# Optimization experiments

Hardware: AMD Instinct MI355X
Metric: run time of the kernel (lower is better)

The kernel has to match this reference:

```python
import jax, jax.numpy as jnp
import numpy as np

B, S, D, H, HD = 2, 4096, 768, 12, 64
W = 256  # one-sided attention window (attention_window=512 // 2)
SCALE = 1.0 / np.sqrt(HD).astype(np.float32)
NEG = -1e9


def setup_inputs() -> dict:
    key = jax.random.key(0)
    ks = jax.random.split(key, 13)
    inp = {"hidden_states": jax.random.normal(ks[0], (B, S, D), dtype=jnp.float32)}
    names = ["Wq", "Wk", "Wv", "Wqg", "Wkg", "Wvg"]
    for i, n in enumerate(names):
        inp[n] = jax.random.normal(ks[1 + i], (D, D), dtype=jnp.float32) * 0.02
        inp["b" + n[1:]] = jax.random.normal(ks[7 + i], (D,), dtype=jnp.float32) * 0.02
    inp["num_global"] = 32
    return inp


def _heads(x):
    # [B,S,D] -> [B,H,S,HD]
    return x.reshape(B, S, H, HD).transpose(0, 2, 1, 3)


def longformer_attn(hidden_states, Wq, bq, Wk, bk, Wv, bv, Wqg, bqg, Wkg, bkg, Wvg, bvg, G):
    q = _heads(hidden_states @ Wq + bq) * SCALE
    k = _heads(hidden_states @ Wk + bk)
    v = _heads(hidden_states @ Wv + bv)

    nc = S // W  # number of query chunks
    # --- banded (sliding window) scores via overlapping key chunks of size 3W ---
    Qc = q.reshape(B, H, nc, W, HD)
    kpad = jnp.pad(k, ((0, 0), (0, 0), (W, W), (0, 0)))
    win_idx = jnp.arange(nc)[:, None] * W + jnp.arange(3 * W)[None, :]  # [nc, 3W]
    K3 = kpad[:, :, win_idx]  # [B,H,nc,3W,HD]
    band = jnp.einsum('bhcqd,bhckd->bhcqk', Qc, K3)  # [B,H,nc,W,3W]
    # mask: key abs position in range, and relative offset within [-W, W]
    c = jnp.arange(nc)[:, None, None]
    pq = jnp.arange(W)[None, :, None]
    e = jnp.arange(3 * W)[None, None, :]
    kabs = c * W + e - W
    valid = (kabs >= 0) & (kabs < S) & (e >= pq) & (e <= pq + 2 * W)
    band = jnp.where(valid[None, None], band, NEG).reshape(B, H, S, 3 * W)

    # --- all queries also attend to the G global keys (regular key proj) ---
    sg = jnp.einsum('bhsd,bhgd->bhsg', q, k[:, :, :G])  # [B,H,S,G]
    probs = jax.nn.softmax(jnp.concatenate([sg, band], axis=-1), axis=-1)
    pg, pb = probs[..., :G], probs[..., G:].reshape(B, H, nc, W, 3 * W)

    vpad = jnp.pad(v, ((0, 0), (0, 0), (W, W), (0, 0)))
    V3 = vpad[:, :, win_idx]  # [B,H,nc,3W,HD]
    out = jnp.einsum('bhcqk,bhckd->bhcqd', pb, V3).reshape(B, H, S, HD)
    out = out + jnp.einsum('bhsg,bhgd->bhsd', pg, v[:, :, :G])

    # --- global queries attend to ALL tokens with the *_global projections ---
    qg = _heads(hidden_states @ Wqg + bqg)[:, :, :G] * SCALE  # [B,H,G,HD]
    kgf = _heads(hidden_states @ Wkg + bkg)
    vgf = _heads(hidden_states @ Wvg + bvg)
    gp = jax.nn.softmax(jnp.einsum('bhgd,bhsd->bhgs', qg, kgf), axis=-1)
    gout = jnp.einsum('bhgs,bhsd->bhgd', gp, vgf)  # [B,H,G,HD]
    out = out.at[:, :, :G].set(gout)

    return out.transpose(0, 2, 1, 3).reshape(B, S, D)


def reference(hidden_states, Wq, bq, Wk, bk, Wv, bv, Wqg, bqg, Wkg, bkg, Wvg, bvg, num_global):
    return longformer_attn(hidden_states, Wq, bq, Wk, bk, Wv, bv, Wqg, bqg, Wkg, bkg, Wvg, bvg, int(num_global))
```

## Files before the change

### kernel.cpp

```cpp
#include <hip/hip_runtime.h>
#include <hip/hip_bf16.h>


#define DEVI __device__ __forceinline__
typedef _Float16 f16;
typedef _Float16 h4 __attribute__((ext_vector_type(4)));
typedef _Float16 f16x8 __attribute__((ext_vector_type(8)));
typedef __attribute__((ext_vector_type(4))) float float4v;

DEVI float4v mfma16(f16x8 a, f16x8 b, float4v c) {
    return __builtin_amdgcn_mfma_f32_16x16x32_f16(a, b, c, 0, 0, 0);
}

DEVI void gl_lds16(const f16* g, f16* l) {
    __builtin_amdgcn_global_load_lds(
        (const __attribute__((address_space(1))) unsigned int*)g,
        (__attribute__((address_space(3))) unsigned int*)l, 16, 0, 0);
}

__global__ __launch_bounds__(256) void xcast(const float* __restrict__ x,
                                             f16* __restrict__ xh) {
    int i = (blockIdx.x * 256 + threadIdx.x) * 4;
    float4 v = *(const float4*)&x[i];
    h4 o = {(f16)v.x, (f16)v.y, (f16)v.z, (f16)v.w};
    *(h4*)&xh[i] = o;
}

__global__ __launch_bounds__(256) void wprep(
    const float* __restrict__ w0, const float* __restrict__ w1,
    const float* __restrict__ w2, const float* __restrict__ w3,
    const float* __restrict__ w4, const float* __restrict__ w5,
    f16* __restrict__ wt) {
    __shared__ float tile[64][65];
    int i = blockIdx.z;
    const float* W = (i == 0) ? w0 : (i == 1) ? w1 : (i == 2) ? w2
                   : (i == 3) ? w3 : (i == 4) ? w4 : w5;
    int n0 = blockIdx.x * 64, k0 = blockIdx.y * 64;
    int tx = threadIdx.x & 63, ty = threadIdx.x >> 6;
#pragma unroll
    for (int yy = 0; yy < 64; yy += 4)
        tile[yy + ty][tx] = W[(size_t)(k0 + yy + ty) * 768 + n0 + tx];
    __syncthreads();
#pragma unroll
    for (int yy = 0; yy < 64; yy += 4)
        wt[(size_t)(i * 768 + n0 + yy + ty) * 768 + k0 + tx] = (f16)tile[tx][yy + ty];
}

__global__ __launch_bounds__(256) void qkv_mfma3(
    const f16* __restrict__ Xh, const f16* __restrict__ Wt,
    const float* __restrict__ b0, const float* __restrict__ b1,
    const float* __restrict__ b2, const float* __restrict__ b3,
    const float* __restrict__ b4, const float* __restrict__ b5,
    f16* __restrict__ q, f16* __restrict__ k, f16* __restrict__ vT,
    f16* __restrict__ qg, f16* __restrict__ kg, f16* __restrict__ vgT) {
    constexpr int CLD = 136;
    __shared__ __align__(16) f16 At[128 * 32];
    __shared__ __align__(16) f16 Bt[128 * 32];
    __shared__ __align__(16) f16 Cl[128 * CLD];
    int tid = threadIdx.x, lane = tid & 63, wid = tid >> 6;
    int quad = lane >> 4, l15 = lane & 15;
    int m0 = blockIdx.x * 128;
    int wm = (wid >> 1) * 64, wn = (wid & 1) * 64;
    const f16* arow0 = Xh + (size_t)m0 * 768;
    const f16* brow0 = Wt + (size_t)blockIdx.y * 128 * 768;

    float4v acc[4][4];
#pragma unroll
    for (int mt = 0; mt < 4; ++mt)
#pragma unroll
        for (int nt = 0; nt < 4; ++nt) acc[mt][nt] = (float4v){0.f, 0.f, 0.f, 0.f};

    int s0 = tid, s1 = tid + 256;
    int r0 = s0 >> 2, o0 = (s0 & 3) * 8;
    int r1 = s1 >> 2, o1 = (s1 & 3) * 8;
    f16* ldsA0 = &At[wid * 512];
    f16* ldsB0 = &Bt[wid * 512];
    f16* ldsA1 = &At[2048 + wid * 512];
    f16* ldsB1 = &Bt[2048 + wid * 512];
    for (int kt = 0; kt < 24; ++kt) {
        int k0 = kt * 32;
        __syncthreads();
        gl_lds16(&arow0[(size_t)r0 * 768 + k0 + o0], ldsA0);
        gl_lds16(&brow0[(size_t)r0 * 768 + k0 + o0], ldsB0);
        gl_lds16(&arow0[(size_t)r1 * 768 + k0 + o1], ldsA1);
        gl_lds16(&brow0[(size_t)r1 * 768 + k0 + o1], ldsB1);
        __syncthreads();
        f16x8 af[4], bf[4];
#pragma unroll
        for (int mt = 0; mt < 4; ++mt)
            af[mt] = *(const f16x8*)&At[(wm + mt * 16 + l15) * 32 + quad * 8];
#pragma unroll
        for (int nt = 0; nt < 4; ++nt)
            bf[nt] = *(const f16x8*)&Bt[(wn + nt * 16 + l15) * 32 + quad * 8];
#pragma unroll
        for (int mt = 0; mt < 4; ++mt)
#pragma unroll
            for (int nt = 0; nt < 4; ++nt) acc[mt][nt] = mfma16(af[mt], bf[nt], acc[mt][nt]);
    }

    int grp = blockIdx.y / 6;
    const float* Bsel = (grp == 0) ? b0 : (grp == 1) ? b1 : (grp == 2) ? b2
                      : (grp == 3) ? b3 : (grp == 4) ? b4 : b5;
    int nb = (blockIdx.y - grp * 6) * 128;
    int b = m0 >> 12;
    bool tr = (grp == 2 || grp == 5);

    if (tr) {
#pragma unroll
        for (int nt = 0; nt < 4; ++nt) {
            float bias = Bsel[nb + wn + nt * 16 + l15];
#pragma unroll
            for (int mt = 0; mt < 4; ++mt) {
                float4v a = acc[mt][nt];
                h4 pk = {(f16)(a[0] + bias), (f16)(a[1] + bias),
                         (f16)(a[2] + bias), (f16)(a[3] + bias)};
                *(h4*)&Cl[(wn + nt * 16 + l15) * CLD + wm + mt * 16 + quad * 4] = pk;
            }
        }
    } else {
        float scale = (grp == 0 || grp == 3) ? 0.125f : 1.0f;
#pragma unroll
        for (int nt = 0; nt < 4; ++nt) {
            float bias = Bsel[nb + wn + nt * 16 + l15];
#pragma unroll
            for (int mt = 0; mt < 4; ++mt) {
                float4v a = acc[mt][nt];
#pragma unroll
                for (int r = 0; r < 4; ++r)
                    Cl[(wm + mt * 16 + quad * 4 + r) * CLD + wn + nt * 16 + l15] =
                        (f16)((a[r] + bias) * scale);
            }
        }
    }
    __syncthreads();

    if (tr) {
        f16* base = (grp == 2) ? vT : vgT;
        int c = tid & 127, sh = (tid >> 7) * 64;
        int ncol = nb + c, h = ncol >> 6, hd = ncol & 63;
        f16* dst = &base[((size_t)((b * 12 + h) * 64 + hd)) * 4096 + (m0 & 4095) + sh];
        const f16* src = &Cl[c * CLD + sh];
#pragma unroll
        for (int i = 0; i < 8; ++i)
            *(f16x8*)&dst[i * 8] = *(const f16x8*)&src[i * 8];
    } else {
        int sl = tid & 127, hh = tid >> 7;
        int s = (m0 & 4095) + sl;
        int h = (nb + hh * 64) >> 6;
        const f16* src = &Cl[sl * CLD + hh * 64];
        f16* dst = nullptr;
        if (grp == 3) {
            if (s < 32) dst = &qg[((size_t)((b * 12 + h) * 32 + s)) * 64];
        } else {
            f16* baseb = (grp == 0) ? q : (grp == 1) ? k : kg;
            dst = &baseb[((size_t)((b * 12 + h) * 4096 + s)) * 64];
        }
        if (dst)
#pragma unroll
            for (int i = 0; i < 8; ++i)
                *(f16x8*)&dst[i * 8] = *(const f16x8*)&src[i * 8];
    }
}

__global__ __launch_bounds__(256, 3) void band_mfma5(
    const f16* __restrict__ q, const f16* __restrict__ k, const f16* __restrict__ vT,
    float* __restrict__ out) {
    constexpr int LDK = 72, LDV = 136, LDP = 40;
    __shared__ __align__(16) f16 Kt[128 * LDK];
    __shared__ __align__(16) f16 Vt[64 * LDV];
    __shared__ __align__(16) f16 Pt[4][32 * LDP];
    int tid = threadIdx.x, lane = tid & 63, wid = tid >> 6;
    int quad = lane >> 4, l15 = lane & 15;
    int c = blockIdx.x & 31, h = (blockIdx.x >> 5) % 12, b = blockIdx.x / 384;
    const f16* qsl = q + (size_t)(b * 12 + h) * 4096 * 64;
    const f16* ksl = k + (size_t)(b * 12 + h) * 4096 * 64;
    const f16* vsl = vT + (size_t)(b * 12 + h) * 64 * 4096;
    int q0 = c * 128;
    int pq0 = q0 + wid * 32;

    f16x8 qf[2][2];
#pragma unroll
    for (int qg = 0; qg < 2; ++qg)
#pragma unroll
        for (int ks = 0; ks < 2; ++ks)
            qf[qg][ks] = *(const f16x8*)&qsl[(size_t)(pq0 + qg * 16 + l15) * 64 +
                                             ks * 32 + quad * 8];

    float4v Ot[4][2];
#pragma unroll
    for (int dt = 0; dt < 4; ++dt)
#pragma unroll
        for (int qg = 0; qg < 2; ++qg) Ot[dt][qg] = (float4v){0.f, 0.f, 0.f, 0.f};
    float lacc[2] = {0.f, 0.f};
    f16* PW = &Pt[wid][0];

    {
#pragma unroll
        for (int jt = 0; jt < 2; ++jt) {
            f16x8 kf0 = *(const f16x8*)&ksl[(size_t)(jt * 16 + l15) * 64 + quad * 8];
            f16x8 kf1 = *(const f16x8*)&ksl[(size_t)(jt * 16 + l15) * 64 + 32 + quad * 8];
#pragma unroll
            for (int qg = 0; qg < 2; ++qg) {
                float4v sacc = (float4v){0.f, 0.f, 0.f, 0.f};
                sacc = mfma16(kf0, qf[qg][0], sacc);
                sacc = mfma16(kf1, qf[qg][1], sacc);
                float p0 = __expf(sacc[0]), p1 = __expf(sacc[1]);
                float p2 = __expf(sacc[2]), p3 = __expf(sacc[3]);
                lacc[qg] += (p0 + p1) + (p2 + p3);
                h4 pk = {(f16)p0, (f16)p1, (f16)p2, (f16)p3};
                *(h4*)&PW[(qg * 16 + l15) * LDP + jt * 16 + quad * 4] = pk;
            }
        }
        f16x8 pf0 = *(const f16x8*)&PW[l15 * LDP + quad * 8];
        f16x8 pf1 = *(const f16x8*)&PW[(16 + l15) * LDP + quad * 8];
#pragma unroll
        for (int dt = 0; dt < 4; ++dt) {
            f16x8 vf = *(const f16x8*)&vsl[(size_t)(dt * 16 + l15) * 4096 + quad * 8];
            Ot[dt][0] = mfma16(vf, pf0, Ot[dt][0]);
            Ot[dt][1] = mfma16(vf, pf1, Ot[dt][1]);
        }
    }

    for (int r = 0; r < 5; ++r) {
        int kb = q0 - 256 + r * 128;
        if (kb < 0 || kb >= 4096) continue;
        __syncthreads();
        {
            int kr = tid >> 1, ko = (tid & 1) * 32;
            const f16* ks2 = &ksl[(size_t)(kb + kr) * 64 + ko];
            f16* kd = &Kt[kr * LDK + ko];
#pragma unroll
            for (int i = 0; i < 4; ++i) *(f16x8*)&kd[i * 8] = *(const f16x8*)&ks2[i * 8];
            int vr = tid >> 2, vo = (tid & 3) * 32;
            const f16* vs2 = &vsl[(size_t)vr * 4096 + kb + vo];
            f16* vd = &Vt[vr * LDV + vo];
#pragma unroll
            for (int i = 0; i < 4; ++i) *(f16x8*)&vd[i * 8] = *(const f16x8*)&vs2[i * 8];
        }
        __syncthreads();

        if (kb + 127 < pq0 - 256 || kb > pq0 + 287) continue;

#pragma unroll
        for (int tt = 0; tt < 2; ++tt) {
            int tb = kb + tt * 64;
            if (tb + 63 < pq0 - 256 || tb > pq0 + 287) continue;
#pragma unroll
            for (int hf = 0; hf < 2; ++hf) {
#pragma unroll
                for (int jt = 0; jt < 2; ++jt) {
                    int jl = tt * 64 + hf * 32 + jt * 16;
                    f16x8 kf0 = *(const f16x8*)&Kt[(jl + l15) * LDK + quad * 8];
                    f16x8 kf1 = *(const f16x8*)&Kt[(jl + l15) * LDK + 32 + quad * 8];
                    int j0 = kb + jl;
#pragma unroll
                    for (int qg = 0; qg < 2; ++qg) {
                        int qlo = pq0 + qg * 16;
                        h4 pk = {(f16)0.f, (f16)0.f, (f16)0.f, (f16)0.f};
                        bool dead = (j0 < qlo - 271) || (j0 > qlo + 271);
                        if (!dead) {
                            float4v sacc = (float4v){0.f, 0.f, 0.f, 0.f};
                            sacc = mfma16(kf0, qf[qg][0], sacc);
                            sacc = mfma16(kf1, qf[qg][1], sacc);
                            float p[4];
                            bool full = (j0 >= qlo - 241) && (j0 <= qlo + 241);
                            if (full) {
#pragma unroll
                                for (int rr = 0; rr < 4; ++rr) p[rr] = __expf(sacc[rr]);
                            } else {
#pragma unroll
                                for (int rr = 0; rr < 4; ++rr) {
                                    int d = (j0 + quad * 4 + rr) - (qlo + l15);
                                    p[rr] = ((unsigned)(d + 256) <= 512u) ? __expf(sacc[rr]) : 0.f;
                                }
                            }
                            lacc[qg] += (p[0] + p[1]) + (p[2] + p[3]);
                            pk = (h4){(f16)p[0], (f16)p[1], (f16)p[2], (f16)p[3]};
                        }
                        *(h4*)&PW[(qg * 16 + l15) * LDP + jt * 16 + quad * 4] = pk;
                    }
                }
                f16x8 pf0 = *(const f16x8*)&PW[l15 * LDP + quad * 8];
                f16x8 pf1 = *(const f16x8*)&PW[(16 + l15) * LDP + quad * 8];
#pragma unroll
                for (int dt = 0; dt < 4; ++dt) {
                    f16x8 vf = *(const f16x8*)&Vt[(dt * 16 + l15) * LDV +
                                                  tt * 64 + hf * 32 + quad * 8];
                    Ot[dt][0] = mfma16(vf, pf0, Ot[dt][0]);
                    Ot[dt][1] = mfma16(vf, pf1, Ot[dt][1]);
                }
            }
        }
    }

#pragma unroll
    for (int qg = 0; qg < 2; ++qg) {
        float lsum = lacc[qg];
        lsum += __shfl_xor(lsum, 16);
        lsum += __shfl_xor(lsum, 32);
        float inv = 1.f / lsum;
        size_t orow = (size_t)(b * 4096 + pq0 + qg * 16 + l15) * 768 + h * 64;
#pragma unroll
        for (int dt = 0; dt < 4; ++dt) {
            float4 o4 = {Ot[dt][qg][0] * inv, Ot[dt][qg][1] * inv,
                         Ot[dt][qg][2] * inv, Ot[dt][qg][3] * inv};
            *(float4*)&out[orow + dt * 16 + quad * 4] = o4;
        }
    }
}

__global__ __launch_bounds__(256) void global_part(
    const f16* __restrict__ qg, const f16* __restrict__ kg, const f16* __restrict__ vgT,
    float* __restrict__ Opart, float* __restrict__ Lpart) {
    constexpr int LDP = 72;
    __shared__ __align__(16) f16 Pt[4][32 * LDP];
    __shared__ __align__(16) float Osh[4][64 * 32];
    __shared__ float Lsh[4][32];
    int tid = threadIdx.x, lane = tid & 63, wid = tid >> 6;
    int quad = lane >> 4, l15 = lane & 15;
    int sl = blockIdx.x & 7, bh = blockIdx.x >> 3;
    const f16* qsl = qg + (size_t)bh * 32 * 64;
    const f16* ksl = kg + (size_t)bh * 4096 * 64;
    const f16* vsl = vgT + (size_t)bh * 64 * 4096;
    int kbase = sl * 512 + wid * 128;

    f16x8 qf[2][2];
#pragma unroll
    for (int g = 0; g < 2; ++g)
#pragma unroll
        for (int ks = 0; ks < 2; ++ks)
            qf[g][ks] = *(const f16x8*)&qsl[(size_t)(g * 16 + l15) * 64 + ks * 32 + quad * 8];

    float4v Ot[4][2];
#pragma unroll
    for (int dt = 0; dt < 4; ++dt)
#pragma unroll
        for (int g = 0; g < 2; ++g) Ot[dt][g] = (float4v){0.f, 0.f, 0.f, 0.f};
    float lacc[2] = {0.f, 0.f};
    f16* PW = &Pt[wid][0];

#pragma unroll
    for (int hf = 0; hf < 2; ++hf) {
        int kh0 = kbase + hf * 64;
#pragma unroll
        for (int kt = 0; kt < 4; ++kt) {
            int jb = kh0 + kt * 16;
            f16x8 kf0 = *(const f16x8*)&ksl[(size_t)(jb + l15) * 64 + quad * 8];
            f16x8 kf1 = *(const f16x8*)&ksl[(size_t)(jb + l15) * 64 + 32 + quad * 8];
#pragma unroll
            for (int g = 0; g < 2; ++g) {
                float4v sacc = (float4v){0.f, 0.f, 0.f, 0.f};
                sacc = mfma16(kf0, qf[g][0], sacc);
                sacc = mfma16(kf1, qf[g][1], sacc);
                float p0 = __expf(sacc[0]), p1 = __expf(sacc[1]);
                float p2 = __expf(sacc[2]), p3 = __expf(sacc[3]);
                lacc[g] += (p0 + p1) + (p2 + p3);
                h4 pk = {(f16)p0, (f16)p1, (f16)p2, (f16)p3};
                *(h4*)&PW[(g * 16 + l15) * LDP + kt * 16 + quad * 4] = pk;
            }
        }
#pragma unroll
        for (int kh = 0; kh < 2; ++kh) {
            f16x8 pf0 = *(const f16x8*)&PW[l15 * LDP + kh * 32 + quad * 8];
            f16x8 pf1 = *(const f16x8*)&PW[(16 + l15) * LDP + kh * 32 + quad * 8];
#pragma unroll
            for (int dt = 0; dt < 4; ++dt) {
                f16x8 vf = *(const f16x8*)&vsl[(size_t)(dt * 16 + l15) * 4096 +
                                               kh0 + kh * 32 + quad * 8];
                Ot[dt][0] = mfma16(vf, pf0, Ot[dt][0]);
                Ot[dt][1] = mfma16(vf, pf1, Ot[dt][1]);
            }
        }
    }

#pragma unroll
    for (int g = 0; g < 2; ++g) {
        lacc[g] += __shfl_xor(lacc[g], 16);
        lacc[g] += __shfl_xor(lacc[g], 32);
    }
    if (quad == 0) { Lsh[wid][l15] = lacc[0]; Lsh[wid][16 + l15] = lacc[1]; }
#pragma unroll
    for (int dt = 0; dt < 4; ++dt)
#pragma unroll
        for (int g = 0; g < 2; ++g)
#pragma unroll
            for (int r = 0; r < 4; ++r)
                Osh[wid][(dt * 16 + quad * 4 + r) * 32 + g * 16 + l15] = Ot[dt][g][r];
    __syncthreads();
#pragma unroll
    for (int i = 0; i < 8; ++i) {
        int idx = tid + i * 256;
        int d = idx & 63, qq = idx >> 6;
        float v = Osh[0][d * 32 + qq] + Osh[1][d * 32 + qq] +
                  Osh[2][d * 32 + qq] + Osh[3][d * 32 + qq];
        Opart[(size_t)blockIdx.x * 2048 + idx] = v;
    }
    if (tid < 32)
        Lpart[blockIdx.x * 32 + tid] = Lsh[0][tid] + Lsh[1][tid] + Lsh[2][tid] + Lsh[3][tid];
}

__global__ __launch_bounds__(256) void global_reduce(
    const float* __restrict__ Opart, const float* __restrict__ Lpart,
    float* __restrict__ out) {
    __shared__ float Ls[32];
    int tid = threadIdx.x, bh = blockIdx.x;
    int b = bh / 12, h = bh % 12;
    if (tid < 32) {
        float s = 0.f;
#pragma unroll
        for (int sl = 0; sl < 8; ++sl) s += Lpart[(bh * 8 + sl) * 32 + tid];
        Ls[tid] = s;
    }
    __syncthreads();
#pragma unroll
    for (int i = 0; i < 8; ++i) {
        int idx = tid + i * 256;
        int d = idx & 63, qq = idx >> 6;
        float o = 0.f;
#pragma unroll
        for (int sl = 0; sl < 8; ++sl) o += Opart[(size_t)(bh * 8 + sl) * 2048 + idx];
        out[(size_t)(b * 4096 + qq) * 768 + h * 64 + d] = o / Ls[qq];
    }
}

extern "C" void kernel_launch(void* const* d_in, const int* in_sizes, int n_in,
                              void* d_out, int out_size, void* d_ws, size_t ws_size,
                              hipStream_t stream) {
    const float* hs = (const float*)d_in[0];
    float* outp = (float*)d_out;

    char* p = (char*)d_ws;
    const size_t SLAB = (size_t)2 * 12 * 4096 * 64 * sizeof(f16);
    f16* qb   = (f16*)(p + 0 * SLAB);
    f16* kb   = (f16*)(p + 1 * SLAB);
    f16* vtb  = (f16*)(p + 2 * SLAB);
    f16* kgb  = (f16*)(p + 3 * SLAB);
    f16* vgtb = (f16*)(p + 4 * SLAB);
    f16* qgb  = (f16*)(p + 5 * SLAB);
    char* p2  = p + 5 * SLAB + 196608;
    f16* xh   = (f16*)p2;
    f16* wt   = (f16*)(p2 + SLAB);
    char* p3  = p2 + SLAB + 7077888;
    float* Opart = (float*)p3;
    float* Lpart = (float*)(p3 + 1572864);

    xcast<<<6144, 256, 0, stream>>>(hs, xh);
    wprep<<<dim3(12, 12, 6), 256, 0, stream>>>(
        (const float*)d_in[1], (const float*)d_in[3], (const float*)d_in[5],
        (const float*)d_in[7], (const float*)d_in[9], (const float*)d_in[11], wt);
    qkv_mfma3<<<dim3(64, 36), 256, 0, stream>>>(
        xh, wt,
        (const float*)d_in[2], (const float*)d_in[4], (const float*)d_in[6],
        (const float*)d_in[8], (const float*)d_in[10], (const float*)d_in[12],
        qb, kb, vtb, qgb, kgb, vgtb);
    band_mfma5<<<768, 256, 0, stream>>>(qb, kb, vtb, outp);
    global_part<<<192, 256, 0, stream>>>(qgb, kgb, vgtb, Opart, Lpart);
    global_reduce<<<24, 256, 0, stream>>>(Opart, Lpart, outp);
}
```

Measured before the change: 236.1 us.

## Merge prep kernels, alias GEMM LDS buffers, skip unused global-query projection tiles

Result: no change. 232.4 us (-1.6%).

```diff
diff --git a/kernel.cpp b/kernel.cpp
--- a/kernel.cpp
+++ b/kernel.cpp
@@ -18,35 +18,37 @@
         (__attribute__((address_space(3))) unsigned int*)l, 16, 0, 0);
 }
 
-__global__ __launch_bounds__(256) void xcast(const float* __restrict__ x,
-                                             f16* __restrict__ xh) {
-    int i = (blockIdx.x * 256 + threadIdx.x) * 4;
-    float4 v = *(const float4*)&x[i];
-    h4 o = {(f16)v.x, (f16)v.y, (f16)v.z, (f16)v.w};
-    *(h4*)&xh[i] = o;
-}
-
-__global__ __launch_bounds__(256) void wprep(
+__global__ __launch_bounds__(256) void prep(
+    const float* __restrict__ x,
     const float* __restrict__ w0, const float* __restrict__ w1,
     const float* __restrict__ w2, const float* __restrict__ w3,
     const float* __restrict__ w4, const float* __restrict__ w5,
-    f16* __restrict__ wt) {
+    f16* __restrict__ xh, f16* __restrict__ wt) {
     __shared__ float tile[64][65];
-    int i = blockIdx.z;
-    const float* W = (i == 0) ? w0 : (i == 1) ? w1 : (i == 2) ? w2
-                   : (i == 3) ? w3 : (i == 4) ? w4 : w5;
-    int n0 = blockIdx.x * 64, k0 = blockIdx.y * 64;
-    int tx = threadIdx.x & 63, ty = threadIdx.x >> 6;
-#pragma unroll
-    for (int yy = 0; yy < 64; yy += 4)
-        tile[yy + ty][tx] = W[(size_t)(k0 + yy + ty) * 768 + n0 + tx];
-    __syncthreads();
-#pragma unroll
-    for (int yy = 0; yy < 64; yy += 4)
-        wt[(size_t)(i * 768 + n0 + yy + ty) * 768 + k0 + tx] = (f16)tile[tx][yy + ty];
-}
-
-__global__ __launch_bounds__(256) void qkv_mfma3(
+    int bid = blockIdx.x;
+    if (bid < 6144) {
+        int i = (bid * 256 + threadIdx.x) * 4;
+        float4 v = *(const float4*)&x[i];
+        h4 o = {(f16)v.x, (f16)v.y, (f16)v.z, (f16)v.w};
+        *(h4*)&xh[i] = o;
+    } else {
+        int t = bid - 6144;
+        int i = t / 144, rem = t - i * 144;
+        int n0 = (rem % 12) * 64, k0 = (rem / 12) * 64;
+        const float* W = (i == 0) ? w0 : (i == 1) ? w1 : (i == 2) ? w2
+                       : (i == 3) ? w3 : (i == 4) ? w4 : w5;
+        int tx = threadIdx.x & 63, ty = threadIdx.x >> 6;
+#pragma unroll
+        for (int yy = 0; yy < 64; yy += 4)
+            tile[yy + ty][tx] = W[(size_t)(k0 + yy + ty) * 768 + n0 + tx];
+        __syncthreads();
+#pragma unroll
+        for (int yy = 0; yy < 64; yy += 4)
+            wt[(size_t)(i * 768 + n0 + yy + ty) * 768 + k0 + tx] = (f16)tile[tx][yy + ty];
+    }
+}
+
+__global__ __launch_bounds__(256) void qkv_mfma4(
     const f16* __restrict__ Xh, const f16* __restrict__ Wt,
     const float* __restrict__ b0, const float* __restrict__ b1,
     const float* __restrict__ b2, const float* __restrict__ b3,
@@ -54,12 +56,15 @@
     f16* __restrict__ q, f16* __restrict__ k, f16* __restrict__ vT,
     f16* __restrict__ qg, f16* __restrict__ kg, f16* __restrict__ vgT) {
     constexpr int CLD = 136;
-    __shared__ __align__(16) f16 At[128 * 32];
-    __shared__ __align__(16) f16 Bt[128 * 32];
-    __shared__ __align__(16) f16 Cl[128 * CLD];
+    __shared__ __align__(16) char smem[128 * CLD * 2];
+    f16* At = (f16*)smem;
+    f16* Bt = (f16*)(smem + 8192);
+    f16* Cl = (f16*)smem;
     int tid = threadIdx.x, lane = tid & 63, wid = tid >> 6;
     int quad = lane >> 4, l15 = lane & 15;
     int m0 = blockIdx.x * 128;
+    int grp = blockIdx.y / 6;
+    if (grp == 3 && (m0 & 4095) != 0) return;
     int wm = (wid >> 1) * 64, wn = (wid & 1) * 64;
     const f16* arow0 = Xh + (size_t)m0 * 768;
     const f16* brow0 = Wt + (size_t)blockIdx.y * 128 * 768;
@@ -97,8 +102,8 @@
 #pragma unroll
             for (int nt = 0; nt < 4; ++nt) acc[mt][nt] = mfma16(af[mt], bf[nt], acc[mt][nt]);
     }
-
-    int grp = blockIdx.y / 6;
+    __syncthreads();
+
     const float* Bsel = (grp == 0) ? b0 : (grp == 1) ? b1 : (grp == 2) ? b2
                       : (grp == 3) ? b3 : (grp == 4) ? b4 : b5;
     int nb = (blockIdx.y - grp * 6) * 128;
@@ -444,11 +449,12 @@
     float* Opart = (float*)p3;
     float* Lpart = (float*)(p3 + 1572864);
 
-    xcast<<<6144, 256, 0, stream>>>(hs, xh);
-    wprep<<<dim3(12, 12, 6), 256, 0, stream>>>(
+    prep<<<7008, 256, 0, stream>>>(
+        hs,
         (const float*)d_in[1], (const float*)d_in[3], (const float*)d_in[5],
-        (const float*)d_in[7], (const float*)d_in[9], (const float*)d_in[11], wt);
-    qkv_mfma3<<<dim3(64, 36), 256, 0, stream>>>(
+        (const float*)d_in[7], (const float*)d_in[9], (const float*)d_in[11],
+        xh, wt);
+    qkv_mfma4<<<dim3(64, 36), 256, 0, stream>>>(
         xh, wt,
         (const float*)d_in[2], (const float*)d_in[4], (const float*)d_in[6],
         (const float*)d_in[8], (const float*)d_in[10], (const float*)d_in[12],
```
